# Kernel optimization log

Measured on AMD Instinct MI355X. Metric: run time of the kernel, lower is better.

The kernel has to match this reference:

```python
import jax, jax.numpy as jnp
import numpy as np

HIDDEN = 768
NUM_HEADS = 12
HEAD_SIZE = HIDDEN // NUM_HEADS
LN_EPS = 1e-5


def setup_inputs() -> dict:
    key = jax.random.key(0)
    ks = jax.random.split(key, 10)
    B, S, H = 2, 4096, HIDDEN
    std = 1.0 / np.sqrt(H)
    inp = {
        "hidden_states": jax.random.normal(ks[0], (B, S, H), dtype=jnp.float32),
        "attention_mask": jnp.ones((B, S), dtype=jnp.float32),
        "Wq": jax.random.normal(ks[1], (H, H), dtype=jnp.float32) * std,
        "bq": jnp.zeros((H,), dtype=jnp.float32),
        "Wk": jax.random.normal(ks[2], (H, H), dtype=jnp.float32) * std,
        "bk": jnp.zeros((H,), dtype=jnp.float32),
        "Wv": jax.random.normal(ks[3], (H, H), dtype=jnp.float32) * std,
        "bv": jnp.zeros((H,), dtype=jnp.float32),
        "Wo": jax.random.normal(ks[4], (H, H), dtype=jnp.float32) * std,
        "bo": jnp.zeros((H,), dtype=jnp.float32),
        "ln_gamma": jnp.ones((H,), dtype=jnp.float32),
        "ln_beta": jnp.zeros((H,), dtype=jnp.float32),
    }
    return inp


def _split_heads(x):
    # [B, S, H] -> [B, nH, S, hd]
    B, S, _ = x.shape
    return x.reshape(B, S, NUM_HEADS, HEAD_SIZE).transpose(0, 2, 1, 3)


def reference(hidden_states, attention_mask, Wq, bq, Wk, bk, Wv, bv, Wo, bo, ln_gamma, ln_beta):
    # QKV projections (torch Linear: x @ W.T + b; here W is stored as [in, out])
    q = _split_heads(hidden_states @ Wq + bq)
    k = _split_heads(hidden_states @ Wk + bk)
    v = _split_heads(hidden_states @ Wv + bv)

    scores = jnp.einsum("bhqd,bhkd->bhqk", q, k) / jnp.sqrt(jnp.float32(HEAD_SIZE))
    # additive mask: (1 - mask) * -10000, broadcast over heads and query positions
    scores = scores + (1.0 - attention_mask)[:, None, None, :] * -10000.0
    probs = jax.nn.softmax(scores, axis=-1)  # dropout_prob = 0 -> identity

    ctx = jnp.einsum("bhqk,bhkd->bhqd", probs, v)
    B, _, S, _ = ctx.shape
    ctx = ctx.transpose(0, 2, 1, 3).reshape(B, S, HIDDEN)

    out = ctx @ Wo + bo
    resid = out + hidden_states
    mu = jnp.mean(resid, axis=-1, keepdims=True)
    var = jnp.var(resid, axis=-1, keepdims=True)
    return (resid - mu) * jax.lax.rsqrt(var + LN_EPS) * ln_gamma + ln_beta
```

## Files before the change

kernel.cpp:

```cpp
#include <hip/hip_runtime.h>
#include <hip/hip_bf16.h>

#define HID 768
#define NHEADS 12
#define HDIM 64
#define SEQ 4096
#define BB 2
#define MTOT (BB * SEQ)

typedef __attribute__((ext_vector_type(8))) short bf16x8;
typedef __attribute__((ext_vector_type(16))) float f32x16;

#define LOG2E 1.4426950408889634f

__device__ inline unsigned pack2bf(float a, float b) {
    __hip_bfloat162 h = __float22bfloat162_rn(float2{a, b});
    return *(unsigned*)&h;
}

__global__ __launch_bounds__(256) void cast_x_kernel(
    const float* __restrict__ X, __hip_bfloat16* __restrict__ Xb)
{
    const size_t i = ((size_t)blockIdx.x * 256 + threadIdx.x) * 8;
    const float4 x0 = *(const float4*)(X + i);
    const float4 x1 = *(const float4*)(X + i + 4);
    unsigned u[4];
    u[0] = pack2bf(x0.x, x0.y);
    u[1] = pack2bf(x0.z, x0.w);
    u[2] = pack2bf(x1.x, x1.y);
    u[3] = pack2bf(x1.z, x1.w);
    *(uint4*)(Xb + i) = *(uint4*)u;
}

__global__ __launch_bounds__(256) void pack_w_kernel(
    const float* __restrict__ Wq, const float* __restrict__ Wk,
    const float* __restrict__ Wv, const float* __restrict__ Wo,
    __hip_bfloat16* __restrict__ Wt)
{
    const int z = blockIdx.z;
    const float* __restrict__ W = (z == 0) ? Wq : (z == 1) ? Wk : (z == 2) ? Wv : Wo;
    const int in0  = blockIdx.x * 64;
    const int out0 = blockIdx.y * 64;
    const int t = threadIdx.x;

    __shared__ float T[64][65];
#pragma unroll
    for (int i = 0; i < 4; ++i) {
        const int idx = t + 256 * i;
        const int row = idx >> 4;
        const int c4  = (idx & 15) << 2;
        const float4 v = *(const float4*)(W + (size_t)(in0 + row) * HID + out0 + c4);
        T[row][c4 + 0] = v.x; T[row][c4 + 1] = v.y;
        T[row][c4 + 2] = v.z; T[row][c4 + 3] = v.w;
    }
    __syncthreads();

    const int o  = t >> 2;
    const int cb = (t & 3) << 4;
    __hip_bfloat16 tmp[16];
#pragma unroll
    for (int k = 0; k < 16; ++k)
        tmp[k] = __float2bfloat16(T[cb + k][o]);
    __hip_bfloat16* __restrict__ dst =
        Wt + (size_t)(z * HID + out0 + o) * HID + in0 + cb;
    *(uint4*)(dst)     = *(uint4*)(&tmp[0]);
    *(uint4*)(dst + 8) = *(uint4*)(&tmp[8]);
}

__global__ __launch_bounds__(256) void qkv_mfma_kernel(
    const __hip_bfloat16* __restrict__ Xb, const __hip_bfloat16* __restrict__ Wt,
    const float* __restrict__ bq, const float* __restrict__ bk,
    const float* __restrict__ bv,
    __hip_bfloat16* __restrict__ Qo, __hip_bfloat16* __restrict__ Ko,
    __hip_bfloat16* __restrict__ Vo)
{
    const int nblk = blockIdx.x;
    const int z  = nblk / 6;
    const int f0 = (nblk % 6) * 128;
    const int n0 = nblk * 128;
    const int m0 = blockIdx.y * 128;

    const float* __restrict__ bias = (z == 0) ? bq : (z == 1) ? bk : bv;

    const int t    = threadIdx.x;
    const int w    = t >> 6;
    const int lane = t & 63;
    const int col  = lane & 31;
    const int g    = lane >> 5;
    const int wm   = w & 1;
    const int wn   = w >> 1;

    __shared__ __hip_bfloat16 smem[2 * 128 * 72];
    __hip_bfloat16 (*As)[72] = (__hip_bfloat16(*)[72])smem;
    __hip_bfloat16 (*Bs)[72] = (__hip_bfloat16(*)[72])(smem + 128 * 72);

    f32x16 acc[2][2];
#pragma unroll
    for (int mt = 0; mt < 2; ++mt)
#pragma unroll
        for (int nt = 0; nt < 2; ++nt)
#pragma unroll
            for (int r = 0; r < 16; ++r) acc[mt][nt][r] = 0.f;

    for (int k0 = 0; k0 < HID; k0 += 64) {
        __syncthreads();
#pragma unroll
        for (int i = 0; i < 4; ++i) {
            const int idx = t + 256 * i;
            const int row = idx >> 3;
            const int c8  = (idx & 7) << 3;
            *(uint4*)&As[row][c8] = *(const uint4*)(Xb + (size_t)(m0 + row) * HID + k0 + c8);
            *(uint4*)&Bs[row][c8] = *(const uint4*)(Wt + (size_t)(n0 + row) * HID + k0 + c8);
        }
        __syncthreads();
#pragma unroll
        for (int kh = 0; kh < 4; ++kh) {
            const int ko = 16 * kh + 8 * g;
            const bf16x8 a0 = *(const bf16x8*)&As[64 * wm + col][ko];
            const bf16x8 a1 = *(const bf16x8*)&As[64 * wm + 32 + col][ko];
            const bf16x8 b0 = *(const bf16x8*)&Bs[64 * wn + col][ko];
            const bf16x8 b1 = *(const bf16x8*)&Bs[64 * wn + 32 + col][ko];
            acc[0][0] = __builtin_amdgcn_mfma_f32_32x32x16_bf16(a0, b0, acc[0][0], 0, 0, 0);
            acc[0][1] = __builtin_amdgcn_mfma_f32_32x32x16_bf16(a0, b1, acc[0][1], 0, 0, 0);
            acc[1][0] = __builtin_amdgcn_mfma_f32_32x32x16_bf16(a1, b0, acc[1][0], 0, 0, 0);
            acc[1][1] = __builtin_amdgcn_mfma_f32_32x32x16_bf16(a1, b1, acc[1][1], 0, 0, 0);
        }
    }

    if (z < 2) {
        __hip_bfloat16* __restrict__ Out = (z == 0) ? Qo : Ko;
        const int h = (f0 >> 6) + wn;
#pragma unroll
        for (int mt = 0; mt < 2; ++mt)
#pragma unroll
            for (int nt = 0; nt < 2; ++nt) {
                const int d = 32 * nt + col;
                const float bsv = bias[f0 + 64 * wn + d];
#pragma unroll
                for (int r = 0; r < 16; ++r) {
                    const int m = m0 + 64 * wm + 32 * mt + (r & 3) + 8 * (r >> 2) + 4 * g;
                    const int b = m >> 12;
                    const int s = m & (SEQ - 1);
                    Out[(((size_t)(b * NHEADS + h)) * SEQ + s) * HDIM + d] =
                        __float2bfloat16(acc[mt][nt][r] + bsv);
                }
            }
    } else {
        __syncthreads();
        __hip_bfloat16 (*Ts)[136] = (__hip_bfloat16(*)[136])smem;
#pragma unroll
        for (int mt = 0; mt < 2; ++mt)
#pragma unroll
            for (int nt = 0; nt < 2; ++nt) {
                const int nloc = 64 * wn + 32 * nt + col;
                const float bsv = bias[f0 + nloc];
#pragma unroll
                for (int rg = 0; rg < 4; ++rg) {
                    const int mbase = 64 * wm + 32 * mt + 8 * rg + 4 * g;
                    unsigned pu[2];
                    pu[0] = pack2bf(acc[mt][nt][4 * rg + 0] + bsv,
                                    acc[mt][nt][4 * rg + 1] + bsv);
                    pu[1] = pack2bf(acc[mt][nt][4 * rg + 2] + bsv,
                                    acc[mt][nt][4 * rg + 3] + bsv);
                    *(uint2*)&Ts[nloc][mbase] = *(uint2*)pu;
                }
            }
        __syncthreads();
        const int nloc = t >> 1;
        const int half = t & 1;
        const int hh = (f0 >> 6) + (nloc >> 6);
        const int d  = nloc & 63;
        const int bb = m0 >> 12;
        const int s0 = m0 & (SEQ - 1);
        __hip_bfloat16* __restrict__ dst =
            Vo + (((size_t)(bb * NHEADS + hh)) * HDIM + d) * SEQ + s0 + 64 * half;
        const __hip_bfloat16* srcp = &Ts[nloc][64 * half];
#pragma unroll
        for (int j = 0; j < 8; ++j)
            *(uint4*)(dst + 8 * j) = *(const uint4*)(srcp + 8 * j);
    }
}

typedef __attribute__((ext_vector_type(2))) unsigned uswap2;

__global__ __launch_bounds__(256, 2) void attn_kernel(
    const __hip_bfloat16* __restrict__ Qb, const __hip_bfloat16* __restrict__ Kb,
    const __hip_bfloat16* __restrict__ Vt, const float* __restrict__ mask,
    __hip_bfloat16* __restrict__ Op, float* __restrict__ lp)
{
    const int bh = blockIdx.y;
    const int b  = bh / NHEADS;
    const int h  = bh - b * NHEADS;
    const int kspan = SEQ / gridDim.z;
    const int kbeg  = blockIdx.z * kspan;

    const int t    = threadIdx.x;
    const int w    = t >> 6;
    const int lane = t & 63;
    const int col  = lane & 31;
    const int g    = lane >> 5;
    const int qw   = blockIdx.x * 256 + 64 * w;

    __shared__ __hip_bfloat16 Ks[64][72];
    __shared__ __hip_bfloat16 Vts[64][72];
    __shared__ float madd[2048];

    const __hip_bfloat16* __restrict__ Qh = Qb + (size_t)bh * SEQ * HDIM;
    const __hip_bfloat16* __restrict__ Kh = Kb + (size_t)bh * SEQ * HDIM;
    const __hip_bfloat16* __restrict__ Vh = Vt + (size_t)bh * HDIM * SEQ;

    for (int j = t; j < kspan; j += 256)
        madd[j] = (1.0f - mask[b * SEQ + kbeg + j]) * (-10000.0f * LOG2E);

    bf16x8 bq[2][4];
#pragma unroll
    for (int mt = 0; mt < 2; ++mt)
#pragma unroll
        for (int kh = 0; kh < 4; ++kh)
            bq[mt][kh] = *(const bf16x8*)(Qh + (size_t)(qw + 32 * mt + col) * HDIM
                                          + 16 * kh + 8 * g);

    f32x16 O[2][2];
    float lac[2] = {0.f, 0.f};
#pragma unroll
    for (int mt = 0; mt < 2; ++mt)
#pragma unroll
        for (int dt = 0; dt < 2; ++dt)
#pragma unroll
            for (int r = 0; r < 16; ++r) O[mt][dt][r] = 0.f;

    const float kscale = 0.125f * LOG2E;

    for (int kt0 = 0; kt0 < kspan; kt0 += 64) {
        const int kt = kbeg + kt0;
        __syncthreads();
#pragma unroll
        for (int i = 0; i < 2; ++i) {
            const int idx = t + 256 * i;
            const int row = idx >> 3;
            const int c8  = (idx & 7) << 3;
            *(uint4*)&Ks[row][c8]  = *(const uint4*)(Kh + (size_t)(kt + row) * HDIM + c8);
            *(uint4*)&Vts[row][c8] = *(const uint4*)(Vh + (size_t)row * SEQ + kt + c8);
        }
        __syncthreads();

        f32x16 St[2][2];
#pragma unroll
        for (int mt = 0; mt < 2; ++mt)
#pragma unroll
            for (int nt = 0; nt < 2; ++nt)
#pragma unroll
                for (int r = 0; r < 16; ++r) St[mt][nt][r] = 0.f;

        __builtin_amdgcn_s_setprio(1);
#pragma unroll
        for (int kh = 0; kh < 4; ++kh) {
            const bf16x8 ak0 = *(const bf16x8*)&Ks[col][16 * kh + 8 * g];
            const bf16x8 ak1 = *(const bf16x8*)&Ks[32 + col][16 * kh + 8 * g];
            St[0][0] = __builtin_amdgcn_mfma_f32_32x32x16_bf16(ak0, bq[0][kh], St[0][0], 0, 0, 0);
            St[1][0] = __builtin_amdgcn_mfma_f32_32x32x16_bf16(ak0, bq[1][kh], St[1][0], 0, 0, 0);
            St[0][1] = __builtin_amdgcn_mfma_f32_32x32x16_bf16(ak1, bq[0][kh], St[0][1], 0, 0, 0);
            St[1][1] = __builtin_amdgcn_mfma_f32_32x32x16_bf16(ak1, bq[1][kh], St[1][1], 0, 0, 0);
        }
        __builtin_amdgcn_s_setprio(0);

#pragma unroll
        for (int mt = 0; mt < 2; ++mt) {
            unsigned g4x[2][4], g4y[2][4];
#pragma unroll
            for (int nt = 0; nt < 2; ++nt) {
#pragma unroll
                for (int b4 = 0; b4 < 4; ++b4) {
                    const float4 mm = *(const float4*)&madd[kt0 + 32 * nt + 8 * b4 + 4 * g];
                    const float p0 = __builtin_amdgcn_exp2f(fmaf(St[mt][nt][4 * b4 + 0], kscale, mm.x));
                    const float p1 = __builtin_amdgcn_exp2f(fmaf(St[mt][nt][4 * b4 + 1], kscale, mm.y));
                    const float p2 = __builtin_amdgcn_exp2f(fmaf(St[mt][nt][4 * b4 + 2], kscale, mm.z));
                    const float p3 = __builtin_amdgcn_exp2f(fmaf(St[mt][nt][4 * b4 + 3], kscale, mm.w));
                    lac[mt] += (p0 + p1) + (p2 + p3);
                    g4x[nt][b4] = pack2bf(p0, p1);
                    g4y[nt][b4] = pack2bf(p2, p3);
                }
            }
#pragma unroll
            for (int kh = 0; kh < 4; ++kh) {
                const int nt  = kh >> 1;
                const int khl = kh & 1;
                union { unsigned u[4]; bf16x8 v; } au;
#if __has_builtin(__builtin_amdgcn_permlane32_swap)
                uswap2 sx = __builtin_amdgcn_permlane32_swap(
                    g4x[nt][2 * khl], g4x[nt][2 * khl + 1], false, false);
                uswap2 sy = __builtin_amdgcn_permlane32_swap(
                    g4y[nt][2 * khl], g4y[nt][2 * khl + 1], false, false);
                au.u[0] = sx[0]; au.u[1] = sy[0]; au.u[2] = sx[1]; au.u[3] = sy[1];
#else
                const unsigned lo_x = g4x[nt][2 * khl],     lo_y = g4y[nt][2 * khl];
                const unsigned hi_x = g4x[nt][2 * khl + 1], hi_y = g4y[nt][2 * khl + 1];
                const unsigned sxv = g ? lo_x : hi_x;
                const unsigned syv = g ? lo_y : hi_y;
                const unsigned rx = (unsigned)__shfl_xor((int)sxv, 32, 64);
                const unsigned ry = (unsigned)__shfl_xor((int)syv, 32, 64);
                if (g) { au.u[0] = rx; au.u[1] = ry; au.u[2] = hi_x; au.u[3] = hi_y; }
                else   { au.u[0] = lo_x; au.u[1] = lo_y; au.u[2] = rx; au.u[3] = ry; }
#endif
                const bf16x8 bv0 = *(const bf16x8*)&Vts[col][16 * kh + 8 * g];
                const bf16x8 bv1 = *(const bf16x8*)&Vts[32 + col][16 * kh + 8 * g];
                __builtin_amdgcn_s_setprio(1);
                O[mt][0] = __builtin_amdgcn_mfma_f32_32x32x16_bf16(au.v, bv0, O[mt][0], 0, 0, 0);
                O[mt][1] = __builtin_amdgcn_mfma_f32_32x32x16_bf16(au.v, bv1, O[mt][1], 0, 0, 0);
                __builtin_amdgcn_s_setprio(0);
            }
        }
    }

    const size_t opbase = (size_t)blockIdx.z * ((size_t)MTOT * HID);
#pragma unroll
    for (int mt = 0; mt < 2; ++mt) {
        const float l = lac[mt] + __shfl_xor(lac[mt], 32, 64);
        if (g == 0)
            lp[((size_t)blockIdx.z * (BB * NHEADS) + bh) * SEQ + qw + 32 * mt + col] = l;
#pragma unroll
        for (int dt = 0; dt < 2; ++dt)
#pragma unroll
            for (int r = 0; r < 16; ++r) {
                const int q = qw + 32 * mt + (r & 3) + 8 * (r >> 2) + 4 * g;
                const int d = 32 * dt + col;
                Op[opbase + ((size_t)b * SEQ + q) * HID + h * HDIM + d] =
                    __float2bfloat16(O[mt][dt][r]);
            }
    }
}

__global__ __launch_bounds__(256) void combine_kernel(
    const __hip_bfloat16* __restrict__ Op, const float* __restrict__ lp,
    __hip_bfloat16* __restrict__ Ctx, int KS)
{
    const size_t i = ((size_t)blockIdx.x * 256 + threadIdx.x) * 8;
    const int n   = (int)(i % HID);
    const int row = (int)(i / HID);
    const int h = n >> 6;
    const int b = row >> 12;
    const int q = row & (SEQ - 1);
    const int bh = b * NHEADS + h;

    float denom = 0.f;
    float o[8] = {};
    for (int kz = 0; kz < KS; ++kz) {
        denom += lp[((size_t)kz * (BB * NHEADS) + bh) * SEQ + q];
        uint4 u = *(const uint4*)(Op + (size_t)kz * ((size_t)MTOT * HID) + i);
        const __hip_bfloat16* e = (const __hip_bfloat16*)&u;
#pragma unroll
        for (int j = 0; j < 8; ++j) o[j] += __bfloat162float(e[j]);
    }
    const float inv = 1.0f / denom;
    unsigned u[4];
#pragma unroll
    for (int j = 0; j < 4; ++j)
        u[j] = pack2bf(o[2 * j] * inv, o[2 * j + 1] * inv);
    *(uint4*)(Ctx + i) = *(uint4*)u;
}

__global__ __launch_bounds__(256) void out_mfma_kernel(
    const __hip_bfloat16* __restrict__ Cb, const __hip_bfloat16* __restrict__ Wto,
    const float* __restrict__ bo, const float* __restrict__ X,
    float* __restrict__ Resid)
{
    const int n0 = blockIdx.x * 128;
    const int m0 = blockIdx.y * 128;

    const int t    = threadIdx.x;
    const int w    = t >> 6;
    const int lane = t & 63;
    const int col  = lane & 31;
    const int g    = lane >> 5;
    const int wm   = w & 1;
    const int wn   = w >> 1;

    __shared__ __hip_bfloat16 As[128][72];
    __shared__ __hip_bfloat16 Bs[128][72];

    f32x16 acc[2][2];
#pragma unroll
    for (int mt = 0; mt < 2; ++mt)
#pragma unroll
        for (int nt = 0; nt < 2; ++nt)
#pragma unroll
            for (int r = 0; r < 16; ++r) acc[mt][nt][r] = 0.f;

    for (int k0 = 0; k0 < HID; k0 += 64) {
        __syncthreads();
#pragma unroll
        for (int i = 0; i < 4; ++i) {
            const int idx = t + 256 * i;
            const int row = idx >> 3;
            const int c8  = (idx & 7) << 3;
            *(uint4*)&As[row][c8] = *(const uint4*)(Cb  + (size_t)(m0 + row) * HID + k0 + c8);
            *(uint4*)&Bs[row][c8] = *(const uint4*)(Wto + (size_t)(n0 + row) * HID + k0 + c8);
        }
        __syncthreads();
#pragma unroll
        for (int kh = 0; kh < 4; ++kh) {
            const int ko = 16 * kh + 8 * g;
            const bf16x8 a0 = *(const bf16x8*)&As[64 * wm + col][ko];
            const bf16x8 a1 = *(const bf16x8*)&As[64 * wm + 32 + col][ko];
            const bf16x8 b0 = *(const bf16x8*)&Bs[64 * wn + col][ko];
            const bf16x8 b1 = *(const bf16x8*)&Bs[64 * wn + 32 + col][ko];
            acc[0][0] = __builtin_amdgcn_mfma_f32_32x32x16_bf16(a0, b0, acc[0][0], 0, 0, 0);
            acc[0][1] = __builtin_amdgcn_mfma_f32_32x32x16_bf16(a0, b1, acc[0][1], 0, 0, 0);
            acc[1][0] = __builtin_amdgcn_mfma_f32_32x32x16_bf16(a1, b0, acc[1][0], 0, 0, 0);
            acc[1][1] = __builtin_amdgcn_mfma_f32_32x32x16_bf16(a1, b1, acc[1][1], 0, 0, 0);
        }
    }

#pragma unroll
    for (int mt = 0; mt < 2; ++mt)
#pragma unroll
        for (int nt = 0; nt < 2; ++nt) {
            const int n = n0 + 64 * wn + 32 * nt + col;
            const float bsv = bo[n];
#pragma unroll
            for (int r = 0; r < 16; ++r) {
                const int m = m0 + 64 * wm + 32 * mt + (r & 3) + 8 * (r >> 2) + 4 * g;
                Resid[(size_t)m * HID + n] = acc[mt][nt][r] + bsv + X[(size_t)m * HID + n];
            }
        }
}

__global__ __launch_bounds__(256) void ln_kernel(
    const float* __restrict__ Rin, const float* __restrict__ gamma,
    const float* __restrict__ beta, float* __restrict__ Out)
{
    const int row = blockIdx.x;
    const int t   = threadIdx.x;
    const float* __restrict__ x = Rin + (size_t)row * HID;

    const float v0 = x[t];
    const float v1 = x[t + 256];
    const float v2 = x[t + 512];
    float s  = v0 + v1 + v2;
    float s2 = v0 * v0 + v1 * v1 + v2 * v2;
#pragma unroll
    for (int off = 32; off; off >>= 1) {
        s  += __shfl_xor(s,  off, 64);
        s2 += __shfl_xor(s2, off, 64);
    }
    __shared__ float rs[4], rs2[4];
    const int w = t >> 6, lane = t & 63;
    if (lane == 0) { rs[w] = s; rs2[w] = s2; }
    __syncthreads();
    const float tot  = rs[0] + rs[1] + rs[2] + rs[3];
    const float tot2 = rs2[0] + rs2[1] + rs2[2] + rs2[3];
    const float mu   = tot * (1.0f / HID);
    const float var  = tot2 * (1.0f / HID) - mu * mu;
    const float rsig = rsqrtf(var + 1e-5f);

    float* __restrict__ y = Out + (size_t)row * HID;
    y[t]       = (v0 - mu) * rsig * gamma[t]       + beta[t];
    y[t + 256] = (v1 - mu) * rsig * gamma[t + 256] + beta[t + 256];
    y[t + 512] = (v2 - mu) * rsig * gamma[t + 512] + beta[t + 512];
}

extern "C" void kernel_launch(void* const* d_in, const int* in_sizes, int n_in,
                              void* d_out, int out_size, void* d_ws, size_t ws_size,
                              hipStream_t stream)
{
    const float* X     = (const float*)d_in[0];
    const float* mask  = (const float*)d_in[1];
    const float* Wq    = (const float*)d_in[2];
    const float* bq    = (const float*)d_in[3];
    const float* Wk    = (const float*)d_in[4];
    const float* bk    = (const float*)d_in[5];
    const float* Wv    = (const float*)d_in[6];
    const float* bv    = (const float*)d_in[7];
    const float* Wo    = (const float*)d_in[8];
    const float* bo    = (const float*)d_in[9];
    const float* gamma = (const float*)d_in[10];
    const float* beta  = (const float*)d_in[11];
    float* out = (float*)d_out;

    const size_t N = (size_t)MTOT * HID;
    const size_t WTE = (size_t)4 * HID * HID;

    char* p = (char*)d_ws;
    __hip_bfloat16* Xb  = (__hip_bfloat16*)p;  p += 2 * N;
    __hip_bfloat16* Wt  = (__hip_bfloat16*)p;  p += 2 * WTE;
    __hip_bfloat16* Qw  = (__hip_bfloat16*)p;  p += 2 * N;
    __hip_bfloat16* Kw  = (__hip_bfloat16*)p;  p += 2 * N;
    __hip_bfloat16* Vtw = (__hip_bfloat16*)p;  p += 2 * N;
    char* opb = p;
    const size_t fixed = (size_t)(opb - (char*)d_ws);

    const size_t lpsz4 = 4 * (size_t)(BB * NHEADS) * SEQ * sizeof(float);
    const int KS = (ws_size >= fixed + 4 * 2 * N + lpsz4) ? 4 : 2;

    __hip_bfloat16* Op  = (__hip_bfloat16*)opb;
    float* lpt = (float*)(opb + (size_t)KS * 2 * N);
    __hip_bfloat16* Ctxb = Xb;
    float* Rd = (float*)Kw;

    cast_x_kernel<<<(int)(N / 2048), 256, 0, stream>>>(X, Xb);
    pack_w_kernel<<<dim3(12, 12, 4), 256, 0, stream>>>(Wq, Wk, Wv, Wo, Wt);
    qkv_mfma_kernel<<<dim3(18, MTOT / 128), 256, 0, stream>>>(
        Xb, Wt, bq, bk, bv, Qw, Kw, Vtw);
    attn_kernel<<<dim3(SEQ / 256, BB * NHEADS, KS), 256, 0, stream>>>(
        Qw, Kw, Vtw, mask, Op, lpt);
    combine_kernel<<<(int)(N / 2048), 256, 0, stream>>>(Op, lpt, Ctxb, KS);
    out_mfma_kernel<<<dim3(6, MTOT / 128), 256, 0, stream>>>(
        Ctxb, Wt + (size_t)2304 * HID, bo, X, Rd);
    ln_kernel<<<MTOT, 256, 0, stream>>>(Rd, gamma, beta, out);
}
```

Baseline: 341.2 us.

## Double-buffer K/V tiles via async global_load_lds with XOR-swizzled LDS

Replaces the synchronous register-staged K/V loads with direct global-to-LDS async loads into two LDS buffers. The next 64-key tile is fetched while the current one is computed. The LDS layout changes from padded rows to an XOR-swizzled 64-wide layout to avoid bank conflicts, and the s_setprio hints are removed. Correctness depends on the global_load_lds per-wave placement matching the swizzle, and on the barrier placement being enough to order the async writes before they are read, since there is no explicit vmcnt wait.

```diff
diff --git a/kernel.cpp b/kernel.cpp
--- a/kernel.cpp
+++ b/kernel.cpp
@@ -201,8 +201,8 @@
     const int g    = lane >> 5;
     const int qw   = blockIdx.x * 256 + 64 * w;
 
-    __shared__ __hip_bfloat16 Ks[64][72];
-    __shared__ __hip_bfloat16 Vts[64][72];
+    __shared__ __hip_bfloat16 Ksb[2][64][64];
+    __shared__ __hip_bfloat16 Vsb[2][64][64];
     __shared__ float madd[2048];
 
     const __hip_bfloat16* __restrict__ Qh = Qb + (size_t)bh * SEQ * HDIM;
@@ -212,6 +212,30 @@
     for (int j = t; j < kspan; j += 256)
         madd[j] = (1.0f - mask[b * SEQ + kbeg + j]) * (-10000.0f * LOG2E);
 
+    const int r0  = t >> 3;
+    const int csw = (((t & 7) ^ (r0 & 7)) << 3);
+
+#define STAGE(BUF, KT) do {                                                        \
+    const __hip_bfloat16* gk0_ = Kh + (size_t)((KT) + r0) * HDIM + csw;            \
+    const __hip_bfloat16* gk1_ = Kh + (size_t)((KT) + r0 + 32) * HDIM + csw;       \
+    const __hip_bfloat16* gv0_ = Vh + (size_t)r0 * SEQ + (KT) + csw;               \
+    const __hip_bfloat16* gv1_ = Vh + (size_t)(r0 + 32) * SEQ + (KT) + csw;        \
+    __hip_bfloat16* lk_ = &Ksb[BUF][0][0] + w * 512;                               \
+    __hip_bfloat16* lv_ = &Vsb[BUF][0][0] + w * 512;                               \
+    __builtin_amdgcn_global_load_lds(                                              \
+        (const __attribute__((address_space(1))) unsigned*)gk0_,                   \
+        (__attribute__((address_space(3))) unsigned*)lk_, 16, 0, 0);               \
+    __builtin_amdgcn_global_load_lds(                                              \
+        (const __attribute__((address_space(1))) unsigned*)gk1_,                   \
+        (__attribute__((address_space(3))) unsigned*)(lk_ + 2048), 16, 0, 0);      \
+    __builtin_amdgcn_global_load_lds(                                              \
+        (const __attribute__((address_space(1))) unsigned*)gv0_,                   \
+        (__attribute__((address_space(3))) unsigned*)lv_, 16, 0, 0);               \
+    __builtin_amdgcn_global_load_lds(                                              \
+        (const __attribute__((address_space(1))) unsigned*)gv1_,                   \
+        (__attribute__((address_space(3))) unsigned*)(lv_ + 2048), 16, 0, 0);      \
+} while (0)
+
     bf16x8 bq[2][4];
 #pragma unroll
     for (int mt = 0; mt < 2; ++mt)
@@ -231,86 +255,88 @@
 
     const float kscale = 0.125f * LOG2E;
 
-    for (int kt0 = 0; kt0 < kspan; kt0 += 64) {
-        const int kt = kbeg + kt0;
-        __syncthreads();
-#pragma unroll
-        for (int i = 0; i < 2; ++i) {
-            const int idx = t + 256 * i;
-            const int row = idx >> 3;
-            const int c8  = (idx & 7) << 3;
-            *(uint4*)&Ks[row][c8]  = *(const uint4*)(Kh + (size_t)(kt + row) * HDIM + c8);
-            *(uint4*)&Vts[row][c8] = *(const uint4*)(Vh + (size_t)row * SEQ + kt + c8);
-        }
-        __syncthreads();
-
-        f32x16 St[2][2];
-#pragma unroll
-        for (int mt = 0; mt < 2; ++mt)
-#pragma unroll
-            for (int nt = 0; nt < 2; ++nt)
-#pragma unroll
-                for (int r = 0; r < 16; ++r) St[mt][nt][r] = 0.f;
-
-        __builtin_amdgcn_s_setprio(1);
-#pragma unroll
-        for (int kh = 0; kh < 4; ++kh) {
-            const bf16x8 ak0 = *(const bf16x8*)&Ks[col][16 * kh + 8 * g];
-            const bf16x8 ak1 = *(const bf16x8*)&Ks[32 + col][16 * kh + 8 * g];
-            St[0][0] = __builtin_amdgcn_mfma_f32_32x32x16_bf16(ak0, bq[0][kh], St[0][0], 0, 0, 0);
-            St[1][0] = __builtin_amdgcn_mfma_f32_32x32x16_bf16(ak0, bq[1][kh], St[1][0], 0, 0, 0);
-            St[0][1] = __builtin_amdgcn_mfma_f32_32x32x16_bf16(ak1, bq[0][kh], St[0][1], 0, 0, 0);
-            St[1][1] = __builtin_amdgcn_mfma_f32_32x32x16_bf16(ak1, bq[1][kh], St[1][1], 0, 0, 0);
-        }
-        __builtin_amdgcn_s_setprio(0);
-
-#pragma unroll
-        for (int mt = 0; mt < 2; ++mt) {
-            unsigned g4x[2][4], g4y[2][4];
-#pragma unroll
-            for (int nt = 0; nt < 2; ++nt) {
-#pragma unroll
-                for (int b4 = 0; b4 < 4; ++b4) {
-                    const float4 mm = *(const float4*)&madd[kt0 + 32 * nt + 8 * b4 + 4 * g];
-                    const float p0 = __builtin_amdgcn_exp2f(fmaf(St[mt][nt][4 * b4 + 0], kscale, mm.x));
-                    const float p1 = __builtin_amdgcn_exp2f(fmaf(St[mt][nt][4 * b4 + 1], kscale, mm.y));
-                    const float p2 = __builtin_amdgcn_exp2f(fmaf(St[mt][nt][4 * b4 + 2], kscale, mm.z));
-                    const float p3 = __builtin_amdgcn_exp2f(fmaf(St[mt][nt][4 * b4 + 3], kscale, mm.w));
-                    lac[mt] += (p0 + p1) + (p2 + p3);
-                    g4x[nt][b4] = pack2bf(p0, p1);
-                    g4y[nt][b4] = pack2bf(p2, p3);
-                }
-            }
-#pragma unroll
-            for (int kh = 0; kh < 4; ++kh) {
-                const int nt  = kh >> 1;
-                const int khl = kh & 1;
-                union { unsigned u[4]; bf16x8 v; } au;
+#define ATTN_TILE(BUF, KT0) do {                                                   \
+    f32x16 St[2][2];                                                               \
+    _Pragma("unroll")                                                              \
+    for (int mt = 0; mt < 2; ++mt)                                                 \
+        _Pragma("unroll")                                                          \
+        for (int nt = 0; nt < 2; ++nt)                                             \
+            _Pragma("unroll")                                                      \
+            for (int r = 0; r < 16; ++r) St[mt][nt][r] = 0.f;                      \
+    _Pragma("unroll")                                                              \
+    for (int kh = 0; kh < 4; ++kh) {                                               \
+        const int sc = ((2 * kh + g) ^ (col & 7)) << 3;                            \
+        const bf16x8 ak0 = *(const bf16x8*)&Ksb[BUF][col][sc];                     \
+        const bf16x8 ak1 = *(const bf16x8*)&Ksb[BUF][32 + col][sc];                \
+        St[0][0] = __builtin_amdgcn_mfma_f32_32x32x16_bf16(ak0, bq[0][kh], St[0][0], 0, 0, 0); \
+        St[1][0] = __builtin_amdgcn_mfma_f32_32x32x16_bf16(ak0, bq[1][kh], St[1][0], 0, 0, 0); \
+        St[0][1] = __builtin_amdgcn_mfma_f32_32x32x16_bf16(ak1, bq[0][kh], St[0][1], 0, 0, 0); \
+        St[1][1] = __builtin_amdgcn_mfma_f32_32x32x16_bf16(ak1, bq[1][kh], St[1][1], 0, 0, 0); \
+    }                                                                              \
+    _Pragma("unroll")                                                              \
+    for (int mt = 0; mt < 2; ++mt) {                                               \
+        unsigned g4x[2][4], g4y[2][4];                                             \
+        _Pragma("unroll")                                                          \
+        for (int nt = 0; nt < 2; ++nt) {                                           \
+            _Pragma("unroll")                                                      \
+            for (int b4 = 0; b4 < 4; ++b4) {                                       \
+                const float4 mm = *(const float4*)&madd[(KT0) + 32 * nt + 8 * b4 + 4 * g]; \
+                const float p0 = __builtin_amdgcn_exp2f(fmaf(St[mt][nt][4 * b4 + 0], kscale, mm.x)); \
+                const float p1 = __builtin_amdgcn_exp2f(fmaf(St[mt][nt][4 * b4 + 1], kscale, mm.y)); \
+                const float p2 = __builtin_amdgcn_exp2f(fmaf(St[mt][nt][4 * b4 + 2], kscale, mm.z)); \
+                const float p3 = __builtin_amdgcn_exp2f(fmaf(St[mt][nt][4 * b4 + 3], kscale, mm.w)); \
+                lac[mt] += (p0 + p1) + (p2 + p3);                                  \
+                g4x[nt][b4] = pack2bf(p0, p1);                                     \
+                g4y[nt][b4] = pack2bf(p2, p3);                                     \
+            }                                                                      \
+        }                                                                          \
+        _Pragma("unroll")                                                          \
+        for (int kh = 0; kh < 4; ++kh) {                                           \
+            const int nt  = kh >> 1;                                               \
+            const int khl = kh & 1;                                                \
+            union { unsigned u[4]; bf16x8 v; } au;                                 \
+            ATTN_PTRANS(au, g4x[nt][2 * khl], g4x[nt][2 * khl + 1],                \
+                            g4y[nt][2 * khl], g4y[nt][2 * khl + 1]);               \
+            const int sc = ((2 * kh + g) ^ (col & 7)) << 3;                        \
+            const bf16x8 bv0 = *(const bf16x8*)&Vsb[BUF][col][sc];                 \
+            const bf16x8 bv1 = *(const bf16x8*)&Vsb[BUF][32 + col][sc];            \
+            O[mt][0] = __builtin_amdgcn_mfma_f32_32x32x16_bf16(au.v, bv0, O[mt][0], 0, 0, 0); \
+            O[mt][1] = __builtin_amdgcn_mfma_f32_32x32x16_bf16(au.v, bv1, O[mt][1], 0, 0, 0); \
+        }                                                                          \
+    }                                                                              \
+} while (0)
+
 #if __has_builtin(__builtin_amdgcn_permlane32_swap)
-                uswap2 sx = __builtin_amdgcn_permlane32_swap(
-                    g4x[nt][2 * khl], g4x[nt][2 * khl + 1], false, false);
-                uswap2 sy = __builtin_amdgcn_permlane32_swap(
-                    g4y[nt][2 * khl], g4y[nt][2 * khl + 1], false, false);
-                au.u[0] = sx[0]; au.u[1] = sy[0]; au.u[2] = sx[1]; au.u[3] = sy[1];
+#define ATTN_PTRANS(au, lox, hix, loy, hiy) do {                                   \
+    uswap2 sx_ = __builtin_amdgcn_permlane32_swap((lox), (hix), false, false);     \
+    uswap2 sy_ = __builtin_amdgcn_permlane32_swap((loy), (hiy), false, false);     \
+    au.u[0] = sx_[0]; au.u[1] = sy_[0]; au.u[2] = sx_[1]; au.u[3] = sy_[1];        \
+} while (0)
 #else
-                const unsigned lo_x = g4x[nt][2 * khl],     lo_y = g4y[nt][2 * khl];
-                const unsigned hi_x = g4x[nt][2 * khl + 1], hi_y = g4y[nt][2 * khl + 1];
-                const unsigned sxv = g ? lo_x : hi_x;
-                const unsigned syv = g ? lo_y : hi_y;
-                const unsigned rx = (unsigned)__shfl_xor((int)sxv, 32, 64);
-                const unsigned ry = (unsigned)__shfl_xor((int)syv, 32, 64);
-                if (g) { au.u[0] = rx; au.u[1] = ry; au.u[2] = hi_x; au.u[3] = hi_y; }
-                else   { au.u[0] = lo_x; au.u[1] = lo_y; au.u[2] = rx; au.u[3] = ry; }
+#define ATTN_PTRANS(au, lox, hix, loy, hiy) do {                                   \
+    const unsigned sxv_ = g ? (lox) : (hix);                                       \
+    const unsigned syv_ = g ? (loy) : (hiy);                                       \
+    const unsigned rx_ = (unsigned)__shfl_xor((int)sxv_, 32, 64);                  \
+    const unsigned ry_ = (unsigned)__shfl_xor((int)syv_, 32, 64);                  \
+    if (g) { au.u[0] = rx_;   au.u[1] = ry_;   au.u[2] = (hix); au.u[3] = (hiy); } \
+    else   { au.u[0] = (lox); au.u[1] = (loy); au.u[2] = rx_;   au.u[3] = ry_;  }  \
+} while (0)
 #endif
-                const bf16x8 bv0 = *(const bf16x8*)&Vts[col][16 * kh + 8 * g];
-                const bf16x8 bv1 = *(const bf16x8*)&Vts[32 + col][16 * kh + 8 * g];
-                __builtin_amdgcn_s_setprio(1);
-                O[mt][0] = __builtin_amdgcn_mfma_f32_32x32x16_bf16(au.v, bv0, O[mt][0], 0, 0, 0);
-                O[mt][1] = __builtin_amdgcn_mfma_f32_32x32x16_bf16(au.v, bv1, O[mt][1], 0, 0, 0);
-                __builtin_amdgcn_s_setprio(0);
-            }
-        }
-    }
+
+    STAGE(0, kbeg);
+    __syncthreads();
+
+    for (int kt0 = 0; kt0 < kspan; kt0 += 128) {
+        STAGE(1, kbeg + kt0 + 64);
+        ATTN_TILE(0, kt0);
+        __syncthreads();
+        if (kt0 + 128 < kspan) STAGE(0, kbeg + kt0 + 128);
+        ATTN_TILE(1, kt0 + 64);
+        __syncthreads();
+    }
+#undef STAGE
+#undef ATTN_TILE
+#undef ATTN_PTRANS
 
     const size_t opbase = (size_t)blockIdx.z * ((size_t)MTOT * HID);
 #pragma unroll
```

Measured after the change: 327.4 us. 4.0% less time.
